# Kernel optimization log

Measured on AMD Instinct MI355X. Metric: run time of the kernel, lower is better.

## Reference

```python
import jax, jax.numpy as jnp
import numpy as np

NEG_SLOPE = 0.2  # PyG GATConv default leaky_relu slope
EPS = 1e-16      # PyG softmax denominator eps


def gat_conv(x, edge_index, W, b, att_src, att_dst, heads, ch, concat):
    """Faithful PyG GATConv (eval mode, self-loops already in edge_index).
    x: [N, F_in]; W: [F_in, heads*ch]; att_src/att_dst: [1, heads, ch]; b: [out]."""
    N = x.shape[0]
    h = (x @ W).reshape(N, heads, ch)                      # [N, H, C]
    a_s = jnp.sum(h * att_src, axis=-1)                    # [N, H]
    a_d = jnp.sum(h * att_dst, axis=-1)                    # [N, H]
    src, dst = edge_index[0], edge_index[1]
    alpha = jax.nn.leaky_relu(a_s[src] + a_d[dst], NEG_SLOPE)  # [E, H]
    # segment softmax over edges grouped by destination node
    amax = jax.ops.segment_max(alpha, dst, num_segments=N)     # [N, H]
    amax = jnp.where(jnp.isfinite(amax), amax, 0.0)
    ex = jnp.exp(alpha - amax[dst])                            # [E, H]
    denom = jax.ops.segment_sum(ex, dst, num_segments=N)       # [N, H]
    alpha = ex / (denom[dst] + EPS)
    msg = alpha[:, :, None] * h[src]                           # [E, H, C]
    out = jax.ops.segment_sum(msg, dst, num_segments=N)        # [N, H, C]
    out = out.reshape(N, heads * ch) if concat else out.mean(axis=1)
    return out + b


def setup_inputs() -> dict:
    key = jax.random.key(0)
    ks = jax.random.split(key, 10)
    N, E, F_in, num_classes = 100000, 1600000, 128, 16
    H1, C1 = 8, 8
    x = jax.random.normal(ks[0], (N, F_in), dtype=jnp.float32)
    edge_index = jax.random.randint(ks[1], (2, E), 0, N, dtype=jnp.int64)
    s1 = (2.0 / (F_in + H1 * C1)) ** 0.5
    W1 = jax.random.normal(ks[2], (F_in, H1 * C1), dtype=jnp.float32) * s1
    b1 = jnp.zeros((H1 * C1,), dtype=jnp.float32)
    att_src1 = jax.random.normal(ks[3], (1, H1, C1), dtype=jnp.float32) * 0.3
    att_dst1 = jax.random.normal(ks[4], (1, H1, C1), dtype=jnp.float32) * 0.3
    s2 = (2.0 / (H1 * C1 + num_classes)) ** 0.5
    W2 = jax.random.normal(ks[5], (H1 * C1, num_classes), dtype=jnp.float32) * s2
    b2 = jnp.zeros((num_classes,), dtype=jnp.float32)
    att_src2 = jax.random.normal(ks[6], (1, 1, num_classes), dtype=jnp.float32) * 0.3
    att_dst2 = jax.random.normal(ks[7], (1, 1, num_classes), dtype=jnp.float32) * 0.3
    return {"x": x, "edge_index": edge_index, "W1": W1, "b1": b1,
            "att_src1": att_src1, "att_dst1": att_dst1,
            "W2": W2, "b2": b2, "att_src2": att_src2, "att_dst2": att_dst2}


def reference(x, edge_index, W1, b1, att_src1, att_dst1, W2, b2, att_src2, att_dst2):
    N = x.shape[0]
    # PyG default add_self_loops=True in both GATConv layers
    loops = jnp.arange(N, dtype=edge_index.dtype)
    ei = jnp.concatenate([edge_index, jnp.stack([loops, loops])], axis=1)
    h = gat_conv(x, ei, W1, b1, att_src1, att_dst1, heads=8, ch=8, concat=True)
    h = jax.nn.elu(h)
    out = gat_conv(h, ei, W2, b2, att_src2, att_dst2, heads=1, ch=16, concat=True)
    return jax.nn.log_softmax(out, axis=1)
```

## Files before the change

kernel.cpp:

```cpp
#include <hip/hip_runtime.h>
#include <hip/hip_bf16.h>


#define NEG_SLOPE 0.2f
#define EPS_DEN 1e-16f
#define CSHIFT 8.0f
#define NBUCK_MAX 256
#define BCAP 16384
#define ECHUNK 2048
#define G1_PITCH 136

typedef __attribute__((ext_vector_type(8))) short bf16x8;
typedef __attribute__((ext_vector_type(4))) float f32x4;

__device__ __forceinline__ float bf2f(unsigned short u) {
    return __uint_as_float(((unsigned)u) << 16);
}
__device__ __forceinline__ unsigned short f2bf(float f) {
    unsigned x = __float_as_uint(f);
    unsigned r = x + 0x7fffu + ((x >> 16) & 1u);
    return (unsigned short)(r >> 16);
}


__global__ __launch_bounds__(256) void bucket_kernel(
    const int* __restrict__ src, const int* __restrict__ dst,
    int* __restrict__ gcur, int* __restrict__ buf, int E, int nbuck)
{
    __shared__ int cnt[NBUCK_MAX];
    __shared__ int offs[NBUCK_MAX];
    int tid = threadIdx.x;
    for (int i = tid; i < nbuck; i += 256) cnt[i] = 0;
    __syncthreads();
    int base = blockIdx.x * ECHUNK;
    int lim = min(base + ECHUNK, E);
    for (int e = base + tid; e < lim; e += 256)
        atomicAdd(&cnt[dst[e] >> 9], 1);
    __syncthreads();
    for (int i = tid; i < nbuck; i += 256) {
        offs[i] = atomicAdd(&gcur[i], cnt[i]);
        cnt[i] = 0;
    }
    __syncthreads();
    for (int e = base + tid; e < lim; e += 256) {
        int d = dst[e];
        int b = d >> 9;
        int idx = offs[b] + atomicAdd(&cnt[b], 1);
        if (idx < BCAP)
            buf[(size_t)b * BCAP + idx] = (src[e] << 9) | (d & 511);
    }
}

__global__ void gscan_kernel(const int* __restrict__ gcur, int* __restrict__ gbase, int B) {
    int lane = threadIdx.x;
    int carry = 0;
    for (int base = 0; base < B; base += 64) {
        int i = base + lane;
        int v = (i < B) ? gcur[i] : 0;
        int sc = v;
#pragma unroll
        for (int off = 1; off < 64; off <<= 1) {
            int o = __shfl_up(sc, off);
            if (lane >= off) sc += o;
        }
        if (i < B) gbase[i] = carry + sc - v;
        carry += __shfl(sc, 63);
    }
}

__global__ __launch_bounds__(256) void csr_bucket_kernel(
    const int* __restrict__ gcur, const int* __restrict__ gbase,
    const int* __restrict__ buf, int* __restrict__ rowptr,
    int* __restrict__ srcs, int N, int E)
{
    __shared__ int cnt[512];
    __shared__ int wsum[4];
    __shared__ int wbase[4];
    int b = blockIdx.x, tid = threadIdx.x;
    int lane = tid & 63, wv = tid >> 6;
    cnt[2 * tid] = 0; cnt[2 * tid + 1] = 0;
    __syncthreads();
    int n = min(gcur[b], BCAP);
    const int* p = buf + (size_t)b * BCAP;
    for (int i = tid; i < n; i += 256) atomicAdd(&cnt[p[i] & 511], 1);
    __syncthreads();
    int c0 = cnt[2 * tid], c1 = cnt[2 * tid + 1];
    int s = c0 + c1;
    int sc = s;
#pragma unroll
    for (int off = 1; off < 64; off <<= 1) {
        int o = __shfl_up(sc, off);
        if (lane >= off) sc += o;
    }
    if (lane == 63) wsum[wv] = sc;
    __syncthreads();
    if (tid == 0) {
        int acc = 0;
#pragma unroll
        for (int k = 0; k < 4; ++k) { wbase[k] = acc; acc += wsum[k]; }
    }
    __syncthreads();
    int base = gbase[b];
    int g0 = base + wbase[wv] + (sc - s);
    int g1 = g0 + c0;
    int node0 = (b << 9) + 2 * tid;
    if (node0 < N)     rowptr[node0]     = g0;
    if (node0 + 1 < N) rowptr[node0 + 1] = g1;
    cnt[2 * tid] = g0; cnt[2 * tid + 1] = g1;
    __syncthreads();
    for (int i = tid; i < n; i += 256) {
        int v = p[i];
        int posi = atomicAdd(&cnt[v & 511], 1);
        srcs[posi] = v >> 9;
    }
    if (b == 0 && tid == 0) rowptr[N] = E;
}


__global__ __launch_bounds__(256) void gemm1_mfma_kernel(
    const float* __restrict__ x, const float* __restrict__ W1,
    const float* __restrict__ att_s, const float* __restrict__ att_d,
    unsigned short* __restrict__ h1b, float* __restrict__ a_s,
    float* __restrict__ a_d, int N)
{
    __shared__ unsigned short As[64 * G1_PITCH];
    __shared__ unsigned short Cs[64 * 68];
    int tid = threadIdx.x;
    int lane = tid & 63, wv = tid >> 6;
    int quad = lane >> 4, l16 = lane & 15;

    bf16x8 Bf[4][4];
#pragma unroll
    for (int ks = 0; ks < 4; ++ks)
#pragma unroll
        for (int nt = 0; nt < 4; ++nt) {
            bf16x8 f;
#pragma unroll
            for (int j = 0; j < 8; ++j)
                f[j] = (short)f2bf(W1[(ks * 32 + quad * 8 + j) * 64 + nt * 16 + l16]);
            Bf[ks][nt] = f;
        }
    float asw[4], adw[4];
#pragma unroll
    for (int nt = 0; nt < 4; ++nt) {
        asw[nt] = att_s[nt * 16 + l16];
        adw[nt] = att_d[nt * 16 + l16];
    }

    int nblocks = (N + 63) >> 6;
    for (int blk = blockIdx.x; blk < nblocks; blk += gridDim.x) {
        int row0 = blk << 6;
        __syncthreads();
#pragma unroll
        for (int i = 0; i < 8; ++i) {
            int idx = tid + 256 * i;
            int r = idx >> 5, c4 = idx & 31;
            int row = row0 + r;
            float4 v = (row < N) ? ((const float4*)x)[(size_t)row * 32 + c4]
                                 : make_float4(0.f, 0.f, 0.f, 0.f);
            ushort4 u;
            u.x = f2bf(v.x); u.y = f2bf(v.y); u.z = f2bf(v.z); u.w = f2bf(v.w);
            *(ushort4*)&As[r * G1_PITCH + c4 * 4] = u;
        }
        __syncthreads();
        f32x4 acc[4];
#pragma unroll
        for (int nt = 0; nt < 4; ++nt) acc[nt] = (f32x4){0.f, 0.f, 0.f, 0.f};
#pragma unroll
        for (int ks = 0; ks < 4; ++ks) {
            bf16x8 Af = *(const bf16x8*)&As[(wv * 16 + l16) * G1_PITCH + ks * 32 + quad * 8];
#pragma unroll
            for (int nt = 0; nt < 4; ++nt)
                acc[nt] = __builtin_amdgcn_mfma_f32_16x16x32_bf16(Af, Bf[ks][nt], acc[nt], 0, 0, 0);
        }
        int lrow = wv * 16 + quad * 4;
#pragma unroll
        for (int nt = 0; nt < 4; ++nt) {
            float ps[4], pd[4];
#pragma unroll
            for (int r = 0; r < 4; ++r) {
                ps[r] = acc[nt][r] * asw[nt];
                pd[r] = acc[nt][r] * adw[nt];
            }
#pragma unroll
            for (int off = 1; off < 8; off <<= 1)
#pragma unroll
                for (int r = 0; r < 4; ++r) {
                    ps[r] += __shfl_xor(ps[r], off);
                    pd[r] += __shfl_xor(pd[r], off);
                }
            if ((l16 & 7) == 0) {
                int head = nt * 2 + (l16 >> 3);
#pragma unroll
                for (int r = 0; r < 4; ++r) {
                    int row = row0 + lrow + r;
                    if (row < N) {
                        a_s[row * 8 + head] = ps[r];
                        a_d[row * 8 + head] = pd[r];
                    }
                }
            }
        }
#pragma unroll
        for (int nt = 0; nt < 4; ++nt)
#pragma unroll
            for (int r = 0; r < 4; ++r)
                Cs[(lrow + r) * 68 + nt * 16 + l16] = f2bf(acc[nt][r]);
        __syncthreads();
#pragma unroll
        for (int i = 0; i < 4; ++i) {
            int idx = tid + 256 * i;
            int r = idx >> 4, c4 = idx & 15;
            int row = row0 + r;
            if (row < N) {
                ushort4 u = *(const ushort4*)&Cs[r * 68 + c4 * 4];
                ((ushort4*)h1b)[(size_t)row * 16 + c4] = u;
            }
        }
    }
}


__global__ __launch_bounds__(256) void agg1_kernel(
    const unsigned short* __restrict__ h1b, const float* __restrict__ a_s,
    const float* __restrict__ a_d, const int* __restrict__ rowptr,
    const int* __restrict__ srcs, const float* __restrict__ b1,
    unsigned short* __restrict__ heb, int N)
{
    int lane = threadIdx.x & 63, wid = threadIdx.x >> 6;
    int node = blockIdx.x * 4 + wid;
    if (node >= N) return;
    int q = lane >> 4, pos = lane & 15, hp = pos >> 1;
    int beg = rowptr[node], end = rowptr[node + 1];
    float adn = a_d[node * 8 + hp];
    const ushort4* h1v = (const ushort4*)h1b;

    float l = 0.f, a0 = 0.f, a1 = 0.f, a2 = 0.f, a3 = 0.f;
    if (q == 0) {
        float v = a_s[node * 8 + hp] + adn;
        v = fmaxf(v, NEG_SLOPE * v);
        float p = __expf(v - CSHIFT);
        ushort4 h = h1v[(size_t)node * 16 + pos];
        l = p;
        a0 = p * bf2f(h.x); a1 = p * bf2f(h.y);
        a2 = p * bf2f(h.z); a3 = p * bf2f(h.w);
    }
    int e = beg + q;
    for (; e + 12 < end; e += 16) {
        int s0 = srcs[e], s1 = srcs[e + 4], s2 = srcs[e + 8], s3 = srcs[e + 12];
        float va0 = a_s[s0 * 8 + hp], va1 = a_s[s1 * 8 + hp];
        float va2 = a_s[s2 * 8 + hp], va3 = a_s[s3 * 8 + hp];
        ushort4 h0 = h1v[(size_t)s0 * 16 + pos];
        ushort4 h1_ = h1v[(size_t)s1 * 16 + pos];
        ushort4 h2_ = h1v[(size_t)s2 * 16 + pos];
        ushort4 h3_ = h1v[(size_t)s3 * 16 + pos];
        float v0 = va0 + adn; v0 = fmaxf(v0, NEG_SLOPE * v0);
        float v1 = va1 + adn; v1 = fmaxf(v1, NEG_SLOPE * v1);
        float v2 = va2 + adn; v2 = fmaxf(v2, NEG_SLOPE * v2);
        float v3 = va3 + adn; v3 = fmaxf(v3, NEG_SLOPE * v3);
        float p0 = __expf(v0 - CSHIFT), p1 = __expf(v1 - CSHIFT);
        float p2 = __expf(v2 - CSHIFT), p3 = __expf(v3 - CSHIFT);
        l += p0 + p1 + p2 + p3;
        a0 = fmaf(p0, bf2f(h0.x), a0); a1 = fmaf(p0, bf2f(h0.y), a1);
        a2 = fmaf(p0, bf2f(h0.z), a2); a3 = fmaf(p0, bf2f(h0.w), a3);
        a0 = fmaf(p1, bf2f(h1_.x), a0); a1 = fmaf(p1, bf2f(h1_.y), a1);
        a2 = fmaf(p1, bf2f(h1_.z), a2); a3 = fmaf(p1, bf2f(h1_.w), a3);
        a0 = fmaf(p2, bf2f(h2_.x), a0); a1 = fmaf(p2, bf2f(h2_.y), a1);
        a2 = fmaf(p2, bf2f(h2_.z), a2); a3 = fmaf(p2, bf2f(h2_.w), a3);
        a0 = fmaf(p3, bf2f(h3_.x), a0); a1 = fmaf(p3, bf2f(h3_.y), a1);
        a2 = fmaf(p3, bf2f(h3_.z), a2); a3 = fmaf(p3, bf2f(h3_.w), a3);
    }
    for (; e < end; e += 4) {
        int s = srcs[e];
        float va = a_s[s * 8 + hp];
        ushort4 h = h1v[(size_t)s * 16 + pos];
        float v = va + adn; v = fmaxf(v, NEG_SLOPE * v);
        float p = __expf(v - CSHIFT);
        l += p;
        a0 = fmaf(p, bf2f(h.x), a0); a1 = fmaf(p, bf2f(h.y), a1);
        a2 = fmaf(p, bf2f(h.z), a2); a3 = fmaf(p, bf2f(h.w), a3);
    }
#pragma unroll
    for (int off = 16; off < 64; off <<= 1) {
        l  += __shfl_xor(l, off);
        a0 += __shfl_xor(a0, off); a1 += __shfl_xor(a1, off);
        a2 += __shfl_xor(a2, off); a3 += __shfl_xor(a3, off);
    }
    if (q == 0) {
        float inv = 1.f / (l + EPS_DEN);
        float4 bb = ((const float4*)b1)[pos];
        float o0 = fmaf(a0, inv, bb.x);
        float o1 = fmaf(a1, inv, bb.y);
        float o2 = fmaf(a2, inv, bb.z);
        float o3 = fmaf(a3, inv, bb.w);
        o0 = o0 > 0.f ? o0 : __expf(o0) - 1.f;
        o1 = o1 > 0.f ? o1 : __expf(o1) - 1.f;
        o2 = o2 > 0.f ? o2 : __expf(o2) - 1.f;
        o3 = o3 > 0.f ? o3 : __expf(o3) - 1.f;
        ushort4 u;
        u.x = f2bf(o0); u.y = f2bf(o1); u.z = f2bf(o2); u.w = f2bf(o3);
        ((ushort4*)heb)[(size_t)node * 16 + pos] = u;
    }
}


__global__ __launch_bounds__(256) void gemm2_kernel(
    const unsigned short* __restrict__ heb, const float* __restrict__ W2,
    const float* __restrict__ att_s2, const float* __restrict__ att_d2,
    unsigned short* __restrict__ h2b, float* __restrict__ a_s2,
    float* __restrict__ a_d2, int N)
{
    __shared__ float xs[4][4 * 68];
    int lane = threadIdx.x & 63, wid = threadIdx.x >> 6;
    int sub = lane >> 4, c = lane & 15;
    float wcol[64];
#pragma unroll
    for (int k = 0; k < 64; ++k) wcol[k] = W2[k * 16 + c];
    float asw = att_s2[c], adw = att_d2[c];
    int groups = (N + 15) >> 4;
    int iters = (groups + gridDim.x - 1) / gridDim.x;
    for (int it = 0; it < iters; ++it) {
        int g = blockIdx.x + it * gridDim.x;
        int nb = g * 16 + wid * 4;
        __syncthreads();
        if (g < groups) {
#pragma unroll
            for (int i = 0; i < 4; ++i) {
                int n = nb + i;
                xs[wid][i * 68 + lane] = (n < N) ? bf2f(heb[(size_t)n * 64 + lane]) : 0.f;
            }
        }
        __syncthreads();
        if (g < groups) {
            int node = nb + sub;
            const float4* xv = (const float4*)&xs[wid][sub * 68];
            float acc = 0.f;
#pragma unroll
            for (int k4 = 0; k4 < 16; ++k4) {
                float4 v = xv[k4];
                acc += v.x * wcol[4 * k4 + 0] + v.y * wcol[4 * k4 + 1]
                     + v.z * wcol[4 * k4 + 2] + v.w * wcol[4 * k4 + 3];
            }
            if (node < N) {
                h2b[(size_t)node * 16 + c] = f2bf(acc);
                float rs = acc * asw, rd = acc * adw;
#pragma unroll
                for (int off = 1; off < 16; off <<= 1) {
                    rs += __shfl_xor(rs, off);
                    rd += __shfl_xor(rd, off);
                }
                if (c == 0) { a_s2[node] = rs; a_d2[node] = rd; }
            }
        }
    }
}


__global__ __launch_bounds__(256) void agg2_kernel(
    const unsigned short* __restrict__ h2b, const float* __restrict__ a_s2,
    const float* __restrict__ a_d2, const int* __restrict__ rowptr,
    const int* __restrict__ srcs, const float* __restrict__ b2,
    float* __restrict__ out, int N)
{
    int lane = threadIdx.x & 63, wid = threadIdx.x >> 6;
    int node = blockIdx.x * 4 + wid;
    if (node >= N) return;
    int q = lane >> 2, pos = lane & 3;
    int beg = rowptr[node], end = rowptr[node + 1];
    float adn = a_d2[node];
    const ushort4* h2v = (const ushort4*)h2b;

    float l = 0.f, a0 = 0.f, a1 = 0.f, a2 = 0.f, a3 = 0.f;
    if (q == 0) {
        float v = a_s2[node] + adn;
        v = fmaxf(v, NEG_SLOPE * v);
        float p = __expf(v - CSHIFT);
        ushort4 h = h2v[(size_t)node * 4 + pos];
        l = p;
        a0 = p * bf2f(h.x); a1 = p * bf2f(h.y);
        a2 = p * bf2f(h.z); a3 = p * bf2f(h.w);
    }
    int e = beg + q;
    for (; e + 16 < end; e += 32) {
        int s0 = srcs[e], s1 = srcs[e + 16];
        float va0 = a_s2[s0], va1 = a_s2[s1];
        ushort4 h0 = h2v[(size_t)s0 * 4 + pos];
        ushort4 h1_ = h2v[(size_t)s1 * 4 + pos];
        float v0 = va0 + adn; v0 = fmaxf(v0, NEG_SLOPE * v0);
        float v1 = va1 + adn; v1 = fmaxf(v1, NEG_SLOPE * v1);
        float p0 = __expf(v0 - CSHIFT), p1 = __expf(v1 - CSHIFT);
        l += p0 + p1;
        a0 = fmaf(p0, bf2f(h0.x), a0); a1 = fmaf(p0, bf2f(h0.y), a1);
        a2 = fmaf(p0, bf2f(h0.z), a2); a3 = fmaf(p0, bf2f(h0.w), a3);
        a0 = fmaf(p1, bf2f(h1_.x), a0); a1 = fmaf(p1, bf2f(h1_.y), a1);
        a2 = fmaf(p1, bf2f(h1_.z), a2); a3 = fmaf(p1, bf2f(h1_.w), a3);
    }
    for (; e < end; e += 16) {
        int s = srcs[e];
        float va = a_s2[s];
        ushort4 h = h2v[(size_t)s * 4 + pos];
        float v = va + adn; v = fmaxf(v, NEG_SLOPE * v);
        float p = __expf(v - CSHIFT);
        l += p;
        a0 = fmaf(p, bf2f(h.x), a0); a1 = fmaf(p, bf2f(h.y), a1);
        a2 = fmaf(p, bf2f(h.z), a2); a3 = fmaf(p, bf2f(h.w), a3);
    }
#pragma unroll
    for (int off = 4; off < 64; off <<= 1) {
        l  += __shfl_xor(l, off);
        a0 += __shfl_xor(a0, off); a1 += __shfl_xor(a1, off);
        a2 += __shfl_xor(a2, off); a3 += __shfl_xor(a3, off);
    }
    if (q == 0) {
        float inv = 1.f / (l + EPS_DEN);
        float4 bb = ((const float4*)b2)[pos];
        float o0 = fmaf(a0, inv, bb.x);
        float o1 = fmaf(a1, inv, bb.y);
        float o2 = fmaf(a2, inv, bb.z);
        float o3 = fmaf(a3, inv, bb.w);
        float mx = fmaxf(fmaxf(o0, o1), fmaxf(o2, o3));
        mx = fmaxf(mx, __shfl_xor(mx, 1));
        mx = fmaxf(mx, __shfl_xor(mx, 2));
        float se = __expf(o0 - mx) + __expf(o1 - mx)
                 + __expf(o2 - mx) + __expf(o3 - mx);
        se += __shfl_xor(se, 1);
        se += __shfl_xor(se, 2);
        float ls = mx + logf(se);
        ((float4*)out)[(size_t)node * 4 + pos] =
            make_float4(o0 - ls, o1 - ls, o2 - ls, o3 - ls);
    }
}


extern "C" void kernel_launch(void* const* d_in, const int* in_sizes, int n_in,
                              void* d_out, int out_size, void* d_ws, size_t ws_size,
                              hipStream_t stream) {
    const float* x    = (const float*)d_in[0];
    const int*   ei   = (const int*)d_in[1];
    const float* W1   = (const float*)d_in[2];
    const float* b1   = (const float*)d_in[3];
    const float* as1  = (const float*)d_in[4];
    const float* ad1  = (const float*)d_in[5];
    const float* W2   = (const float*)d_in[6];
    const float* b2   = (const float*)d_in[7];
    const float* as2  = (const float*)d_in[8];
    const float* ad2  = (const float*)d_in[9];
    float* out = (float*)d_out;

    int N = in_sizes[0] / 128;
    int E = in_sizes[1] / 2;
    const int* srcp = ei;
    const int* dstp = ei + E;
    int nbuck = (N + 511) >> 9;

    char* w = (char*)d_ws;
    auto alloc = [&](size_t bytes) {
        void* p = (void*)w;
        w += (bytes + 255) & ~(size_t)255;
        return p;
    };
    unsigned short* h1b = (unsigned short*)alloc((size_t)N * 64 * 2);
    float* a_s1  = (float*)alloc((size_t)N * 8 * 4);
    float* a_d1  = (float*)alloc((size_t)N * 8 * 4);
    unsigned short* heb = (unsigned short*)alloc((size_t)N * 64 * 2);
    unsigned short* h2b = (unsigned short*)alloc((size_t)N * 16 * 2);
    float* a_s2b = (float*)alloc((size_t)N * 4);
    float* a_d2b = (float*)alloc((size_t)N * 4);
    int*   rowp  = (int*)alloc((size_t)(N + 1) * 4);
    int*   srcs  = (int*)alloc((size_t)E * 4);
    int*   gcur  = (int*)alloc((size_t)nbuck * 4);
    int*   gbase = (int*)alloc((size_t)nbuck * 4);
    int*   buf   = (int*)alloc((size_t)nbuck * BCAP * 4);

    hipMemsetAsync(gcur, 0, (size_t)nbuck * 4, stream);

    int bblk = (E + ECHUNK - 1) / ECHUNK;
    bucket_kernel<<<bblk, 256, 0, stream>>>(srcp, dstp, gcur, buf, E, nbuck);
    gscan_kernel<<<1, 64, 0, stream>>>(gcur, gbase, nbuck);
    csr_bucket_kernel<<<nbuck, 256, 0, stream>>>(gcur, gbase, buf, rowp, srcs, N, E);

    int g1blocks = (N + 63) >> 6;
    gemm1_mfma_kernel<<<g1blocks, 256, 0, stream>>>(x, W1, as1, ad1, h1b, a_s1, a_d1, N);
    agg1_kernel<<<(N + 3) / 4, 256, 0, stream>>>(h1b, a_s1, a_d1, rowp, srcs, b1, heb, N);
    gemm2_kernel<<<512, 256, 0, stream>>>(heb, W2, as2, ad2, h2b, a_s2b, a_d2b, N);
    agg2_kernel<<<(N + 3) / 4, 256, 0, stream>>>(h2b, a_s2b, a_d2b, rowp, srcs, b2, out, N);
}
```

Baseline: 296.9 us.

## Fuse bucketing with GEMM1, fold scan into last block, fuse GEMM2 into agg1

Bucketing and the first GEMM now run as one launch using separate block ranges. The last bucketing block to finish, found through an atomic counter, performs the global scan, so the separate scan kernel is gone. Buckets shrink to 256 nodes with a smaller capacity. The layer-2 projection and attention logits are computed inside agg1, which removes the heb intermediate and the gemm2 launch. Both aggregation kernels switch to 16-byte per-lane loads with wider per-lane feature slices. The risks are bucket overflow from the smaller BCAP and extra W2 reads per node in agg1.

```diff
diff --git a/kernel.cpp b/kernel.cpp
--- a/kernel.cpp
+++ b/kernel.cpp
@@ -5,8 +5,7 @@
 #define NEG_SLOPE 0.2f
 #define EPS_DEN 1e-16f
 #define CSHIFT 8.0f
-#define NBUCK_MAX 256
-#define BCAP 16384
+#define BCAP 8192
 #define ECHUNK 2048
 #define G1_PITCH 136
 
@@ -21,136 +20,109 @@
     unsigned r = x + 0x7fffu + ((x >> 16) & 1u);
     return (unsigned short)(r >> 16);
 }
-
-
-__global__ __launch_bounds__(256) void bucket_kernel(
+__device__ __forceinline__ void bf2f2(unsigned u, float& lo, float& hi) {
+    lo = __uint_as_float(u << 16);
+    hi = __uint_as_float(u & 0xffff0000u);
+}
+__device__ __forceinline__ void acc8(float* a, float p, uint4 h) {
+    float f0, f1;
+    bf2f2(h.x, f0, f1); a[0] = fmaf(p, f0, a[0]); a[1] = fmaf(p, f1, a[1]);
+    bf2f2(h.y, f0, f1); a[2] = fmaf(p, f0, a[2]); a[3] = fmaf(p, f1, a[3]);
+    bf2f2(h.z, f0, f1); a[4] = fmaf(p, f0, a[4]); a[5] = fmaf(p, f1, a[5]);
+    bf2f2(h.w, f0, f1); a[6] = fmaf(p, f0, a[6]); a[7] = fmaf(p, f1, a[7]);
+}
+
+union __align__(16) SMem {
+    struct { unsigned short As[64 * G1_PITCH]; unsigned short Cs[64 * 68]; } g;
+    struct { int cnt[512]; int offs[512]; int flag; } b;
+};
+
+
+__global__ __launch_bounds__(256) void bucket_gemm1_kernel(
     const int* __restrict__ src, const int* __restrict__ dst,
-    int* __restrict__ gcur, int* __restrict__ buf, int E, int nbuck)
-{
-    __shared__ int cnt[NBUCK_MAX];
-    __shared__ int offs[NBUCK_MAX];
-    int tid = threadIdx.x;
-    for (int i = tid; i < nbuck; i += 256) cnt[i] = 0;
-    __syncthreads();
-    int base = blockIdx.x * ECHUNK;
-    int lim = min(base + ECHUNK, E);
-    for (int e = base + tid; e < lim; e += 256)
-        atomicAdd(&cnt[dst[e] >> 9], 1);
-    __syncthreads();
-    for (int i = tid; i < nbuck; i += 256) {
-        offs[i] = atomicAdd(&gcur[i], cnt[i]);
-        cnt[i] = 0;
-    }
-    __syncthreads();
-    for (int e = base + tid; e < lim; e += 256) {
-        int d = dst[e];
-        int b = d >> 9;
-        int idx = offs[b] + atomicAdd(&cnt[b], 1);
-        if (idx < BCAP)
-            buf[(size_t)b * BCAP + idx] = (src[e] << 9) | (d & 511);
-    }
-}
-
-__global__ void gscan_kernel(const int* __restrict__ gcur, int* __restrict__ gbase, int B) {
-    int lane = threadIdx.x;
-    int carry = 0;
-    for (int base = 0; base < B; base += 64) {
-        int i = base + lane;
-        int v = (i < B) ? gcur[i] : 0;
-        int sc = v;
-#pragma unroll
-        for (int off = 1; off < 64; off <<= 1) {
-            int o = __shfl_up(sc, off);
-            if (lane >= off) sc += o;
-        }
-        if (i < B) gbase[i] = carry + sc - v;
-        carry += __shfl(sc, 63);
-    }
-}
-
-__global__ __launch_bounds__(256) void csr_bucket_kernel(
-    const int* __restrict__ gcur, const int* __restrict__ gbase,
-    const int* __restrict__ buf, int* __restrict__ rowptr,
-    int* __restrict__ srcs, int N, int E)
-{
-    __shared__ int cnt[512];
-    __shared__ int wsum[4];
-    __shared__ int wbase[4];
-    int b = blockIdx.x, tid = threadIdx.x;
-    int lane = tid & 63, wv = tid >> 6;
-    cnt[2 * tid] = 0; cnt[2 * tid + 1] = 0;
-    __syncthreads();
-    int n = min(gcur[b], BCAP);
-    const int* p = buf + (size_t)b * BCAP;
-    for (int i = tid; i < n; i += 256) atomicAdd(&cnt[p[i] & 511], 1);
-    __syncthreads();
-    int c0 = cnt[2 * tid], c1 = cnt[2 * tid + 1];
-    int s = c0 + c1;
-    int sc = s;
-#pragma unroll
-    for (int off = 1; off < 64; off <<= 1) {
-        int o = __shfl_up(sc, off);
-        if (lane >= off) sc += o;
-    }
-    if (lane == 63) wsum[wv] = sc;
-    __syncthreads();
-    if (tid == 0) {
-        int acc = 0;
-#pragma unroll
-        for (int k = 0; k < 4; ++k) { wbase[k] = acc; acc += wsum[k]; }
-    }
-    __syncthreads();
-    int base = gbase[b];
-    int g0 = base + wbase[wv] + (sc - s);
-    int g1 = g0 + c0;
-    int node0 = (b << 9) + 2 * tid;
-    if (node0 < N)     rowptr[node0]     = g0;
-    if (node0 + 1 < N) rowptr[node0 + 1] = g1;
-    cnt[2 * tid] = g0; cnt[2 * tid + 1] = g1;
-    __syncthreads();
-    for (int i = tid; i < n; i += 256) {
-        int v = p[i];
-        int posi = atomicAdd(&cnt[v & 511], 1);
-        srcs[posi] = v >> 9;
-    }
-    if (b == 0 && tid == 0) rowptr[N] = E;
-}
-
-
-__global__ __launch_bounds__(256) void gemm1_mfma_kernel(
+    int* __restrict__ gcur, int* __restrict__ gbase, int* __restrict__ buf,
+    int E, int nbuck, int bblk,
     const float* __restrict__ x, const float* __restrict__ W1,
     const float* __restrict__ att_s, const float* __restrict__ att_d,
     unsigned short* __restrict__ h1b, float* __restrict__ a_s,
     float* __restrict__ a_d, int N)
 {
-    __shared__ unsigned short As[64 * G1_PITCH];
-    __shared__ unsigned short Cs[64 * 68];
+    __shared__ SMem sm;
     int tid = threadIdx.x;
-    int lane = tid & 63, wv = tid >> 6;
-    int quad = lane >> 4, l16 = lane & 15;
-
-    bf16x8 Bf[4][4];
-#pragma unroll
-    for (int ks = 0; ks < 4; ++ks)
+    if ((int)blockIdx.x < bblk) {
+        int* cnt = sm.b.cnt; int* offs = sm.b.offs;
+        for (int i = tid; i < nbuck; i += 256) cnt[i] = 0;
+        __syncthreads();
+        int base = blockIdx.x * ECHUNK;
+        int lim = min(base + ECHUNK, E);
+        int dl[8];
+#pragma unroll
+        for (int k = 0; k < 8; ++k) {
+            int e = base + tid + 256 * k;
+            dl[k] = (e < lim) ? dst[e] : -1;
+        }
+#pragma unroll
+        for (int k = 0; k < 8; ++k)
+            if (dl[k] >= 0) atomicAdd(&cnt[dl[k] >> 8], 1);
+        __syncthreads();
+        for (int i = tid; i < nbuck; i += 256) {
+            offs[i] = atomicAdd(&gcur[i], cnt[i]);
+            cnt[i] = 0;
+        }
+        __syncthreads();
+#pragma unroll
+        for (int k = 0; k < 8; ++k) {
+            if (dl[k] >= 0) {
+                int e = base + tid + 256 * k;
+                int b = dl[k] >> 8;
+                int idx = offs[b] + atomicAdd(&cnt[b], 1);
+                if (idx < BCAP)
+                    buf[(size_t)b * BCAP + idx] = (src[e] << 8) | (dl[k] & 255);
+            }
+        }
+        __threadfence();
+        __syncthreads();
+        if (tid == 0) sm.b.flag = (atomicAdd(&gcur[nbuck], 1) == bblk - 1) ? 1 : 0;
+        __syncthreads();
+        if (sm.b.flag && tid < 64) {
+            int lane = tid, carry = 0;
+            for (int bs = 0; bs < nbuck; bs += 64) {
+                int i = bs + lane;
+                int v = (i < nbuck) ? atomicAdd(&gcur[i], 0) : 0;
+                int sc = v;
+#pragma unroll
+                for (int off = 1; off < 64; off <<= 1) {
+                    int o = __shfl_up(sc, off);
+                    if (lane >= off) sc += o;
+                }
+                if (i < nbuck) gbase[i] = carry + sc - v;
+                carry += __shfl(sc, 63);
+            }
+        }
+    } else {
+        unsigned short* As = sm.g.As;
+        unsigned short* Cs = sm.g.Cs;
+        int bb = blockIdx.x - bblk;
+        int lane = tid & 63, wv = tid >> 6;
+        int quad = lane >> 4, l16 = lane & 15;
+        bf16x8 Bf[4][4];
+#pragma unroll
+        for (int ks = 0; ks < 4; ++ks)
+#pragma unroll
+            for (int nt = 0; nt < 4; ++nt) {
+                bf16x8 f;
+#pragma unroll
+                for (int j = 0; j < 8; ++j)
+                    f[j] = (short)f2bf(W1[(ks * 32 + quad * 8 + j) * 64 + nt * 16 + l16]);
+                Bf[ks][nt] = f;
+            }
+        float asw[4], adw[4];
 #pragma unroll
         for (int nt = 0; nt < 4; ++nt) {
-            bf16x8 f;
-#pragma unroll
-            for (int j = 0; j < 8; ++j)
-                f[j] = (short)f2bf(W1[(ks * 32 + quad * 8 + j) * 64 + nt * 16 + l16]);
-            Bf[ks][nt] = f;
-        }
-    float asw[4], adw[4];
-#pragma unroll
-    for (int nt = 0; nt < 4; ++nt) {
-        asw[nt] = att_s[nt * 16 + l16];
-        adw[nt] = att_d[nt * 16 + l16];
-    }
-
-    int nblocks = (N + 63) >> 6;
-    for (int blk = blockIdx.x; blk < nblocks; blk += gridDim.x) {
-        int row0 = blk << 6;
-        __syncthreads();
+            asw[nt] = att_s[nt * 16 + l16];
+            adw[nt] = att_d[nt * 16 + l16];
+        }
+        int row0 = bb << 6;
 #pragma unroll
         for (int i = 0; i < 8; ++i) {
             int idx = tid + 256 * i;
@@ -221,138 +193,137 @@
 }
 
 
-__global__ __launch_bounds__(256) void agg1_kernel(
+__global__ __launch_bounds__(256) void csr_bucket_kernel(
+    const int* __restrict__ gcur, const int* __restrict__ gbase,
+    const int* __restrict__ buf, int* __restrict__ rowptr,
+    int* __restrict__ srcs, int N, int E)
+{
+    __shared__ int cnt[256];
+    __shared__ int wsum[4];
+    __shared__ int wbase[4];
+    int b = blockIdx.x, tid = threadIdx.x;
+    int lane = tid & 63, wv = tid >> 6;
+    cnt[tid] = 0;
+    __syncthreads();
+    int n = min(gcur[b], BCAP);
+    const int* p = buf + (size_t)b * BCAP;
+    for (int i = tid; i < n; i += 256) atomicAdd(&cnt[p[i] & 255], 1);
+    __syncthreads();
+    int c = cnt[tid];
+    int sc = c;
+#pragma unroll
+    for (int off = 1; off < 64; off <<= 1) {
+        int o = __shfl_up(sc, off);
+        if (lane >= off) sc += o;
+    }
+    if (lane == 63) wsum[wv] = sc;
+    __syncthreads();
+    if (tid == 0) {
+        int acc = 0;
+#pragma unroll
+        for (int k = 0; k < 4; ++k) { wbase[k] = acc; acc += wsum[k]; }
+    }
+    __syncthreads();
+    int excl = gbase[b] + wbase[wv] + (sc - c);
+    int node = (b << 8) + tid;
+    if (node < N) rowptr[node] = excl;
+    cnt[tid] = excl;
+    __syncthreads();
+    for (int i = tid; i < n; i += 256) {
+        int v = p[i];
+        int posi = atomicAdd(&cnt[v & 255], 1);
+        srcs[posi] = v >> 8;
+    }
+    if (b == 0 && tid == 0) rowptr[N] = E;
+}
+
+
+__global__ __launch_bounds__(256) void agg1_fused_kernel(
     const unsigned short* __restrict__ h1b, const float* __restrict__ a_s,
     const float* __restrict__ a_d, const int* __restrict__ rowptr,
     const int* __restrict__ srcs, const float* __restrict__ b1,
-    unsigned short* __restrict__ heb, int N)
+    const float* __restrict__ W2, const float* __restrict__ att_s2,
+    const float* __restrict__ att_d2, unsigned short* __restrict__ h2b,
+    float* __restrict__ a_s2, float* __restrict__ a_d2, int N)
 {
     int lane = threadIdx.x & 63, wid = threadIdx.x >> 6;
     int node = blockIdx.x * 4 + wid;
     if (node >= N) return;
-    int q = lane >> 4, pos = lane & 15, hp = pos >> 1;
+    int g = lane >> 3, pos = lane & 7;
     int beg = rowptr[node], end = rowptr[node + 1];
-    float adn = a_d[node * 8 + hp];
-    const ushort4* h1v = (const ushort4*)h1b;
-
-    float l = 0.f, a0 = 0.f, a1 = 0.f, a2 = 0.f, a3 = 0.f;
-    if (q == 0) {
-        float v = a_s[node * 8 + hp] + adn;
+    float adn = a_d[node * 8 + pos];
+    const uint4* h1v = (const uint4*)h1b;
+
+    float l = 0.f, a[8] = {0.f, 0.f, 0.f, 0.f, 0.f, 0.f, 0.f, 0.f};
+    if (g == 0) {
+        float v = a_s[node * 8 + pos] + adn;
         v = fmaxf(v, NEG_SLOPE * v);
         float p = __expf(v - CSHIFT);
-        ushort4 h = h1v[(size_t)node * 16 + pos];
         l = p;
-        a0 = p * bf2f(h.x); a1 = p * bf2f(h.y);
-        a2 = p * bf2f(h.z); a3 = p * bf2f(h.w);
-    }
-    int e = beg + q;
-    for (; e + 12 < end; e += 16) {
-        int s0 = srcs[e], s1 = srcs[e + 4], s2 = srcs[e + 8], s3 = srcs[e + 12];
-        float va0 = a_s[s0 * 8 + hp], va1 = a_s[s1 * 8 + hp];
-        float va2 = a_s[s2 * 8 + hp], va3 = a_s[s3 * 8 + hp];
-        ushort4 h0 = h1v[(size_t)s0 * 16 + pos];
-        ushort4 h1_ = h1v[(size_t)s1 * 16 + pos];
-        ushort4 h2_ = h1v[(size_t)s2 * 16 + pos];
-        ushort4 h3_ = h1v[(size_t)s3 * 16 + pos];
+        acc8(a, p, h1v[(size_t)node * 8 + pos]);
+    }
+    int e = beg + g;
+    for (; e + 8 < end; e += 16) {
+        int s0 = srcs[e], s1 = srcs[e + 8];
+        float va0 = a_s[s0 * 8 + pos], va1 = a_s[s1 * 8 + pos];
+        uint4 h0 = h1v[(size_t)s0 * 8 + pos];
+        uint4 h1_ = h1v[(size_t)s1 * 8 + pos];
         float v0 = va0 + adn; v0 = fmaxf(v0, NEG_SLOPE * v0);
         float v1 = va1 + adn; v1 = fmaxf(v1, NEG_SLOPE * v1);
-        float v2 = va2 + adn; v2 = fmaxf(v2, NEG_SLOPE * v2);
-        float v3 = va3 + adn; v3 = fmaxf(v3, NEG_SLOPE * v3);
         float p0 = __expf(v0 - CSHIFT), p1 = __expf(v1 - CSHIFT);
-        float p2 = __expf(v2 - CSHIFT), p3 = __expf(v3 - CSHIFT);
-        l += p0 + p1 + p2 + p3;
-        a0 = fmaf(p0, bf2f(h0.x), a0); a1 = fmaf(p0, bf2f(h0.y), a1);
-        a2 = fmaf(p0, bf2f(h0.z), a2); a3 = fmaf(p0, bf2f(h0.w), a3);
-        a0 = fmaf(p1, bf2f(h1_.x), a0); a1 = fmaf(p1, bf2f(h1_.y), a1);
-        a2 = fmaf(p1, bf2f(h1_.z), a2); a3 = fmaf(p1, bf2f(h1_.w), a3);
-        a0 = fmaf(p2, bf2f(h2_.x), a0); a1 = fmaf(p2, bf2f(h2_.y), a1);
-        a2 = fmaf(p2, bf2f(h2_.z), a2); a3 = fmaf(p2, bf2f(h2_.w), a3);
-        a0 = fmaf(p3, bf2f(h3_.x), a0); a1 = fmaf(p3, bf2f(h3_.y), a1);
-        a2 = fmaf(p3, bf2f(h3_.z), a2); a3 = fmaf(p3, bf2f(h3_.w), a3);
-    }
-    for (; e < end; e += 4) {
+        l += p0 + p1;
+        acc8(a, p0, h0);
+        acc8(a, p1, h1_);
+    }
+    if (e < end) {
         int s = srcs[e];
-        float va = a_s[s * 8 + hp];
-        ushort4 h = h1v[(size_t)s * 16 + pos];
+        float va = a_s[s * 8 + pos];
+        uint4 h = h1v[(size_t)s * 8 + pos];
         float v = va + adn; v = fmaxf(v, NEG_SLOPE * v);
         float p = __expf(v - CSHIFT);
         l += p;
-        a0 = fmaf(p, bf2f(h.x), a0); a1 = fmaf(p, bf2f(h.y), a1);
-        a2 = fmaf(p, bf2f(h.z), a2); a3 = fmaf(p, bf2f(h.w), a3);
-    }
-#pragma unroll
-    for (int off = 16; off < 64; off <<= 1) {
-        l  += __shfl_xor(l, off);
-        a0 += __shfl_xor(a0, off); a1 += __shfl_xor(a1, off);
-        a2 += __shfl_xor(a2, off); a3 += __shfl_xor(a3, off);
-    }
-    if (q == 0) {
-        float inv = 1.f / (l + EPS_DEN);
-        float4 bb = ((const float4*)b1)[pos];
-        float o0 = fmaf(a0, inv, bb.x);
-        float o1 = fmaf(a1, inv, bb.y);
-        float o2 = fmaf(a2, inv, bb.z);
-        float o3 = fmaf(a3, inv, bb.w);
-        o0 = o0 > 0.f ? o0 : __expf(o0) - 1.f;
-        o1 = o1 > 0.f ? o1 : __expf(o1) - 1.f;
-        o2 = o2 > 0.f ? o2 : __expf(o2) - 1.f;
-        o3 = o3 > 0.f ? o3 : __expf(o3) - 1.f;
-        ushort4 u;
-        u.x = f2bf(o0); u.y = f2bf(o1); u.z = f2bf(o2); u.w = f2bf(o3);
-        ((ushort4*)heb)[(size_t)node * 16 + pos] = u;
-    }
-}
-
-
-__global__ __launch_bounds__(256) void gemm2_kernel(
-    const unsigned short* __restrict__ heb, const float* __restrict__ W2,
-    const float* __restrict__ att_s2, const float* __restrict__ att_d2,
-    unsigned short* __restrict__ h2b, float* __restrict__ a_s2,
-    float* __restrict__ a_d2, int N)
-{
-    __shared__ float xs[4][4 * 68];
-    int lane = threadIdx.x & 63, wid = threadIdx.x >> 6;
-    int sub = lane >> 4, c = lane & 15;
-    float wcol[64];
-#pragma unroll
-    for (int k = 0; k < 64; ++k) wcol[k] = W2[k * 16 + c];
-    float asw = att_s2[c], adw = att_d2[c];
-    int groups = (N + 15) >> 4;
-    int iters = (groups + gridDim.x - 1) / gridDim.x;
-    for (int it = 0; it < iters; ++it) {
-        int g = blockIdx.x + it * gridDim.x;
-        int nb = g * 16 + wid * 4;
-        __syncthreads();
-        if (g < groups) {
-#pragma unroll
-            for (int i = 0; i < 4; ++i) {
-                int n = nb + i;
-                xs[wid][i * 68 + lane] = (n < N) ? bf2f(heb[(size_t)n * 64 + lane]) : 0.f;
-            }
-        }
-        __syncthreads();
-        if (g < groups) {
-            int node = nb + sub;
-            const float4* xv = (const float4*)&xs[wid][sub * 68];
-            float acc = 0.f;
-#pragma unroll
-            for (int k4 = 0; k4 < 16; ++k4) {
-                float4 v = xv[k4];
-                acc += v.x * wcol[4 * k4 + 0] + v.y * wcol[4 * k4 + 1]
-                     + v.z * wcol[4 * k4 + 2] + v.w * wcol[4 * k4 + 3];
-            }
-            if (node < N) {
-                h2b[(size_t)node * 16 + c] = f2bf(acc);
-                float rs = acc * asw, rd = acc * adw;
-#pragma unroll
-                for (int off = 1; off < 16; off <<= 1) {
-                    rs += __shfl_xor(rs, off);
-                    rd += __shfl_xor(rd, off);
-                }
-                if (c == 0) { a_s2[node] = rs; a_d2[node] = rd; }
-            }
-        }
-    }
+        acc8(a, p, h);
+    }
+#pragma unroll
+    for (int off = 8; off < 64; off <<= 1) {
+        l += __shfl_xor(l, off);
+#pragma unroll
+        for (int j = 0; j < 8; ++j) a[j] += __shfl_xor(a[j], off);
+    }
+    float inv = 1.f / (l + EPS_DEN);
+    float4 bb0 = ((const float4*)b1)[pos * 2];
+    float4 bb1 = ((const float4*)b1)[pos * 2 + 1];
+    float o[8];
+    o[0] = fmaf(a[0], inv, bb0.x); o[1] = fmaf(a[1], inv, bb0.y);
+    o[2] = fmaf(a[2], inv, bb0.z); o[3] = fmaf(a[3], inv, bb0.w);
+    o[4] = fmaf(a[4], inv, bb1.x); o[5] = fmaf(a[5], inv, bb1.y);
+    o[6] = fmaf(a[6], inv, bb1.z); o[7] = fmaf(a[7], inv, bb1.w);
+#pragma unroll
+    for (int j = 0; j < 8; ++j)
+        o[j] = o[j] > 0.f ? o[j] : __expf(o[j]) - 1.f;
+
+    float r0 = 0.f, r1 = 0.f;
+#pragma unroll
+    for (int j = 0; j < 8; ++j) {
+        float2 w = ((const float2*)W2)[(8 * pos + j) * 8 + g];
+        r0 = fmaf(o[j], w.x, r0);
+        r1 = fmaf(o[j], w.y, r1);
+    }
+    r0 += __shfl_xor(r0, 1); r1 += __shfl_xor(r1, 1);
+    r0 += __shfl_xor(r0, 2); r1 += __shfl_xor(r1, 2);
+    r0 += __shfl_xor(r0, 4); r1 += __shfl_xor(r1, 4);
+    float2 ws = ((const float2*)att_s2)[g];
+    float2 wd = ((const float2*)att_d2)[g];
+    float ps = r0 * ws.x + r1 * ws.y;
+    float pd = r0 * wd.x + r1 * wd.y;
+    ps += __shfl_xor(ps, 8);  pd += __shfl_xor(pd, 8);
+    ps += __shfl_xor(ps, 16); pd += __shfl_xor(pd, 16);
+    ps += __shfl_xor(ps, 32); pd += __shfl_xor(pd, 32);
+    if (pos == 0) {
+        ushort2 u; u.x = f2bf(r0); u.y = f2bf(r1);
+        ((ushort2*)h2b)[(size_t)node * 8 + g] = u;
+    }
+    if (lane == 0) { a_s2[node] = ps; a_d2[node] = pd; }
 }
 
 
@@ -365,69 +336,56 @@
     int lane = threadIdx.x & 63, wid = threadIdx.x >> 6;
     int node = blockIdx.x * 4 + wid;
     if (node >= N) return;
-    int q = lane >> 2, pos = lane & 3;
+    int g = lane >> 1, pos = lane & 1;
     int beg = rowptr[node], end = rowptr[node + 1];
     float adn = a_d2[node];
-    const ushort4* h2v = (const ushort4*)h2b;
-
-    float l = 0.f, a0 = 0.f, a1 = 0.f, a2 = 0.f, a3 = 0.f;
-    if (q == 0) {
+    const uint4* h2v = (const uint4*)h2b;
+
+    float l = 0.f, a[8] = {0.f, 0.f, 0.f, 0.f, 0.f, 0.f, 0.f, 0.f};
+    if (g == 0) {
         float v = a_s2[node] + adn;
         v = fmaxf(v, NEG_SLOPE * v);
         float p = __expf(v - CSHIFT);
-        ushort4 h = h2v[(size_t)node * 4 + pos];
         l = p;
-        a0 = p * bf2f(h.x); a1 = p * bf2f(h.y);
-        a2 = p * bf2f(h.z); a3 = p * bf2f(h.w);
-    }
-    int e = beg + q;
-    for (; e + 16 < end; e += 32) {
-        int s0 = srcs[e], s1 = srcs[e + 16];
-        float va0 = a_s2[s0], va1 = a_s2[s1];
-        ushort4 h0 = h2v[(size_t)s0 * 4 + pos];
-        ushort4 h1_ = h2v[(size_t)s1 * 4 + pos];
-        float v0 = va0 + adn; v0 = fmaxf(v0, NEG_SLOPE * v0);
-        float v1 = va1 + adn; v1 = fmaxf(v1, NEG_SLOPE * v1);
-        float p0 = __expf(v0 - CSHIFT), p1 = __expf(v1 - CSHIFT);
-        l += p0 + p1;
-        a0 = fmaf(p0, bf2f(h0.x), a0); a1 = fmaf(p0, bf2f(h0.y), a1);
-        a2 = fmaf(p0, bf2f(h0.z), a2); a3 = fmaf(p0, bf2f(h0.w), a3);
-        a0 = fmaf(p1, bf2f(h1_.x), a0); a1 = fmaf(p1, bf2f(h1_.y), a1);
-        a2 = fmaf(p1, bf2f(h1_.z), a2); a3 = fmaf(p1, bf2f(h1_.w), a3);
-    }
-    for (; e < end; e += 16) {
+        acc8(a, p, h2v[(size_t)node * 2 + pos]);
+    }
+    for (int e = beg + g; e < end; e += 32) {
         int s = srcs[e];
         float va = a_s2[s];
-        ushort4 h = h2v[(size_t)s * 4 + pos];
+        uint4 h = h2v[(size_t)s * 2 + pos];
         float v = va + adn; v = fmaxf(v, NEG_SLOPE * v);
         float p = __expf(v - CSHIFT);
         l += p;
-        a0 = fmaf(p, bf2f(h.x), a0); a1 = fmaf(p, bf2f(h.y), a1);
-        a2 = fmaf(p, bf2f(h.z), a2); a3 = fmaf(p, bf2f(h.w), a3);
-    }
-#pragma unroll
-    for (int off = 4; off < 64; off <<= 1) {
-        l  += __shfl_xor(l, off);
-        a0 += __shfl_xor(a0, off); a1 += __shfl_xor(a1, off);
-        a2 += __shfl_xor(a2, off); a3 += __shfl_xor(a3, off);
-    }
-    if (q == 0) {
-        float inv = 1.f / (l + EPS_DEN);
-        float4 bb = ((const float4*)b2)[pos];
-        float o0 = fmaf(a0, inv, bb.x);
-        float o1 = fmaf(a1, inv, bb.y);
-        float o2 = fmaf(a2, inv, bb.z);
-        float o3 = fmaf(a3, inv, bb.w);
-        float mx = fmaxf(fmaxf(o0, o1), fmaxf(o2, o3));
-        mx = fmaxf(mx, __shfl_xor(mx, 1));
-        mx = fmaxf(mx, __shfl_xor(mx, 2));
-        float se = __expf(o0 - mx) + __expf(o1 - mx)
-                 + __expf(o2 - mx) + __expf(o3 - mx);
-        se += __shfl_xor(se, 1);
-        se += __shfl_xor(se, 2);
-        float ls = mx + logf(se);
-        ((float4*)out)[(size_t)node * 4 + pos] =
-            make_float4(o0 - ls, o1 - ls, o2 - ls, o3 - ls);
+        acc8(a, p, h);
+    }
+#pragma unroll
+    for (int off = 2; off < 64; off <<= 1) {
+        l += __shfl_xor(l, off);
+#pragma unroll
+        for (int j = 0; j < 8; ++j) a[j] += __shfl_xor(a[j], off);
+    }
+    float inv = 1.f / (l + EPS_DEN);
+    float4 bb0 = ((const float4*)b2)[pos * 2];
+    float4 bb1 = ((const float4*)b2)[pos * 2 + 1];
+    float o[8];
+    o[0] = fmaf(a[0], inv, bb0.x); o[1] = fmaf(a[1], inv, bb0.y);
+    o[2] = fmaf(a[2], inv, bb0.z); o[3] = fmaf(a[3], inv, bb0.w);
+    o[4] = fmaf(a[4], inv, bb1.x); o[5] = fmaf(a[5], inv, bb1.y);
+    o[6] = fmaf(a[6], inv, bb1.z); o[7] = fmaf(a[7], inv, bb1.w);
+    float mx = o[0];
+#pragma unroll
+    for (int j = 1; j < 8; ++j) mx = fmaxf(mx, o[j]);
+    mx = fmaxf(mx, __shfl_xor(mx, 1));
+    float se = 0.f;
+#pragma unroll
+    for (int j = 0; j < 8; ++j) se += __expf(o[j] - mx);
+    se += __shfl_xor(se, 1);
+    float ls = mx + logf(se);
+    if (g == 0) {
+        ((float4*)out)[(size_t)node * 4 + pos * 2] =
+            make_float4(o[0] - ls, o[1] - ls, o[2] - ls, o[3] - ls);
+        ((float4*)out)[(size_t)node * 4 + pos * 2 + 1] =
+            make_float4(o[4] - ls, o[5] - ls, o[6] - ls, o[7] - ls);
     }
 }
 
@@ -451,7 +409,7 @@
     int E = in_sizes[1] / 2;
     const int* srcp = ei;
     const int* dstp = ei + E;
-    int nbuck = (N + 511) >> 9;
+    int nbuck = (N + 255) >> 8;
 
     char* w = (char*)d_ws;
     auto alloc = [&](size_t bytes) {
@@ -462,26 +420,24 @@
     unsigned short* h1b = (unsigned short*)alloc((size_t)N * 64 * 2);
     float* a_s1  = (float*)alloc((size_t)N * 8 * 4);
     float* a_d1  = (float*)alloc((size_t)N * 8 * 4);
-    unsigned short* heb = (unsigned short*)alloc((size_t)N * 64 * 2);
     unsigned short* h2b = (unsigned short*)alloc((size_t)N * 16 * 2);
     float* a_s2b = (float*)alloc((size_t)N * 4);
     float* a_d2b = (float*)alloc((size_t)N * 4);
     int*   rowp  = (int*)alloc((size_t)(N + 1) * 4);
     int*   srcs  = (int*)alloc((size_t)E * 4);
-    int*   gcur  = (int*)alloc((size_t)nbuck * 4);
+    int*   gcur  = (int*)alloc((size_t)(nbuck + 1) * 4);
     int*   gbase = (int*)alloc((size_t)nbuck * 4);
     int*   buf   = (int*)alloc((size_t)nbuck * BCAP * 4);
 
-    hipMemsetAsync(gcur, 0, (size_t)nbuck * 4, stream);
+    hipMemsetAsync(gcur, 0, (size_t)(nbuck + 1) * 4, stream);
 
     int bblk = (E + ECHUNK - 1) / ECHUNK;
-    bucket_kernel<<<bblk, 256, 0, stream>>>(srcp, dstp, gcur, buf, E, nbuck);
-    gscan_kernel<<<1, 64, 0, stream>>>(gcur, gbase, nbuck);
+    int g1blocks = (N + 63) >> 6;
+    bucket_gemm1_kernel<<<bblk + g1blocks, 256, 0, stream>>>(
+        srcp, dstp, gcur, gbase, buf, E, nbuck, bblk,
+        x, W1, as1, ad1, h1b, a_s1, a_d1, N);
     csr_bucket_kernel<<<nbuck, 256, 0, stream>>>(gcur, gbase, buf, rowp, srcs, N, E);
-
-    int g1blocks = (N + 63) >> 6;
-    gemm1_mfma_kernel<<<g1blocks, 256, 0, stream>>>(x, W1, as1, ad1, h1b, a_s1, a_d1, N);
-    agg1_kernel<<<(N + 3) / 4, 256, 0, stream>>>(h1b, a_s1, a_d1, rowp, srcs, b1, heb, N);
-    gemm2_kernel<<<512, 256, 0, stream>>>(heb, W2, as2, ad2, h2b, a_s2b, a_d2b, N);
+    agg1_fused_kernel<<<(N + 3) / 4, 256, 0, stream>>>(
+        h1b, a_s1, a_d1, rowp, srcs, b1, W2, as2, ad2, h2b, a_s2b, a_d2b, N);
     agg2_kernel<<<(N + 3) / 4, 256, 0, stream>>>(h2b, a_s2b, a_d2b, rowp, srcs, b2, out, N);
 }
```

New measurement: 465.7 us. 1.57x slower.
